# Performance work log

Measured on AMD Instinct MI355X. Metric: run time of the kernel, lower is better.

## Reference

```python
import jax, jax.numpy as jnp
import numpy as np

NUM_NODES = 100000
NUM_FEATURES = 64
HIDDEN = 128
NUM_CLASSES = 2
N_CLIQUES = 500000
CLIQUE_SIZE = 4


def setup_inputs() -> dict:
    key = jax.random.key(0)
    k = jax.random.split(key, 8)
    x = jax.random.normal(k[0], (NUM_NODES, NUM_FEATURES), dtype=jnp.float32)
    cliques_r = jax.random.randint(k[1], (N_CLIQUES, CLIQUE_SIZE), 0, NUM_NODES)
    cliques_s = jax.random.randint(k[2], (N_CLIQUES, CLIQUE_SIZE), 0, NUM_NODES)
    # learned parameters
    node_features = jax.random.normal(k[3], (NUM_NODES, NUM_FEATURES), dtype=jnp.float32)
    W5 = jax.random.normal(k[4], (NUM_FEATURES, HIDDEN), dtype=jnp.float32) / np.sqrt(NUM_FEATURES)
    b5 = jnp.zeros((HIDDEN,), dtype=jnp.float32)
    W6 = jax.random.normal(k[5], (HIDDEN, NUM_CLASSES), dtype=jnp.float32) / np.sqrt(HIDDEN)
    b6 = jnp.zeros((NUM_CLASSES,), dtype=jnp.float32)
    return {"x": x, "cliques_r": cliques_r, "cliques_s": cliques_s,
            "node_features": node_features, "W5": W5, "b5": b5, "W6": W6, "b6": b6}


def _edge_pred(node_features, cliques, W5, b5, W6, b6):
    # EdgePredNet: edge_index = positions 0..k-1, so x_i = clique node 0, x_j = clique node 1.
    x_i = node_features[cliques[:, 0]]  # [N, F] irregular gather
    x_j = node_features[cliques[:, 1]]  # [N, F]
    h = jax.nn.relu((x_i * x_j) @ W5 + b5)  # [N, H]
    logits = h @ W6 + b6  # [N, C]
    return jax.nn.softmax(logits, axis=-1)


def reference(x, cliques_r, cliques_s, node_features, W5, b5, W6, b6):
    # forward ignores the x argument: x = self.node_features
    probs_r = _edge_pred(node_features, cliques_r, W5, b5, W6, b6)           # [Nr, C]
    probs_s = _edge_pred(node_features, cliques_s, W5, b5, W6, b6)[:, None]  # [Ns, 1, C] (stacked singleton lists)
    return probs_r, probs_s
```

## Files before the change

### kernel.cpp

```cpp
#include <hip/hip_runtime.h>
#include <hip/hip_bf16.h>
#include <hip/hip_fp16.h>

typedef _Float16 half8 __attribute__((ext_vector_type(8)));
typedef float    f32x4 __attribute__((ext_vector_type(4)));

#define NCLQ      500000
#define NF        64
#define HID       128
#define NTILES    62500
#define RTILES    31250
#define NFH_ELEMS 6400000

__global__ __launch_bounds__(256) void cvt_kernel(const float* __restrict__ nf,
                                                  const float* __restrict__ w5,
                                                  _Float16* __restrict__ nfh,
                                                  _Float16* __restrict__ w5h)
{
    const long id = (long)blockIdx.x * blockDim.x + threadIdx.x;
    const long NCHUNK = NFH_ELEMS / 8;
    const long WCHUNK = (NF * HID) / 8;
    const float* src; _Float16* dst; long c;
    if (id < NCHUNK)                { src = nf; dst = nfh; c = id; }
    else if (id < NCHUNK + WCHUNK)  { src = w5; dst = w5h; c = id - NCHUNK; }
    else return;
    const float4 u = ((const float4*)src)[c * 2 + 0];
    const float4 v = ((const float4*)src)[c * 2 + 1];
    half8 h;
    h[0] = (_Float16)u.x; h[1] = (_Float16)u.y; h[2] = (_Float16)u.z; h[3] = (_Float16)u.w;
    h[4] = (_Float16)v.x; h[5] = (_Float16)v.y; h[6] = (_Float16)v.z; h[7] = (_Float16)v.w;
    ((half8*)dst)[c] = h;
}

template <int PRE>
__global__ __launch_bounds__(256, 4) void edge_pred_kernel(
    const float*    __restrict__ nf,
    const _Float16* __restrict__ nfh,
    const int*      __restrict__ cr,
    const int*      __restrict__ cs,
    const float*    __restrict__ w5,
    const _Float16* __restrict__ w5h,
    const float*    __restrict__ b5,
    const float*    __restrict__ w6,
    const float*    __restrict__ b6,
    float*          __restrict__ out)
{
    const int lane = threadIdx.x & 63;
    const int wid  = threadIdx.x >> 6;
    const int i    = lane & 15;
    const int g    = lane >> 4;

    half8 bfrag[8][2];
    float b5r[8], wdr[8];
#pragma unroll
    for (int t = 0; t < 8; ++t) {
        const int col = 16 * t + i;
        b5r[t] = b5[col];
        wdr[t] = w6[2 * col] - w6[2 * col + 1];
#pragma unroll
        for (int kb = 0; kb < 2; ++kb) {
            half8 f;
#pragma unroll
            for (int e = 0; e < 8; ++e) {
                const int k = 32 * kb + 8 * g + e;
                f[e] = PRE ? w5h[k * HID + col] : (_Float16)w5[k * HID + col];
            }
            bfrag[t][kb] = f;
        }
    }
    const float bdiff = b6[0] - b6[1];

    const int gw = blockIdx.x * 4 + wid;
    const int nw = gridDim.x * 4;
    if (gw >= NTILES) return;

    auto clq = [&](int T) -> int2 {
        T = (T < NTILES) ? T : (NTILES - 1);
        const bool is_r = (T < RTILES);
        const int* cl   = is_r ? cr : cs;
        const long e    = (long)(is_r ? T : T - RTILES) * 16 + i;
        return *(const int2*)(cl + e * 4);
    };
    auto gather = [&](int2 idx, half8& d0a, half8& d0b, half8& d1a, half8& d1b) {
        if constexpr (PRE) {
            const _Float16* p0 = nfh + (long)idx.x * NF;
            const _Float16* p1 = nfh + (long)idx.y * NF;
            d0a = *(const half8*)(p0 + 8 * g);
            d0b = *(const half8*)(p0 + 32 + 8 * g);
            d1a = *(const half8*)(p1 + 8 * g);
            d1b = *(const half8*)(p1 + 32 + 8 * g);
        } else {
            const float* p0 = nf + (long)idx.x * NF;
            const float* p1 = nf + (long)idx.y * NF;
            const float4 xa = *(const float4*)(p0 + 8 * g);
            const float4 xb = *(const float4*)(p0 + 8 * g + 4);
            const float4 ya = *(const float4*)(p1 + 8 * g);
            const float4 yb = *(const float4*)(p1 + 8 * g + 4);
            const float4 xc = *(const float4*)(p0 + 32 + 8 * g);
            const float4 xd = *(const float4*)(p0 + 32 + 8 * g + 4);
            const float4 yc = *(const float4*)(p1 + 32 + 8 * g);
            const float4 yd = *(const float4*)(p1 + 32 + 8 * g + 4);
            d0a[0]=(_Float16)xa.x; d0a[1]=(_Float16)xa.y; d0a[2]=(_Float16)xa.z; d0a[3]=(_Float16)xa.w;
            d0a[4]=(_Float16)xb.x; d0a[5]=(_Float16)xb.y; d0a[6]=(_Float16)xb.z; d0a[7]=(_Float16)xb.w;
            d0b[0]=(_Float16)xc.x; d0b[1]=(_Float16)xc.y; d0b[2]=(_Float16)xc.z; d0b[3]=(_Float16)xc.w;
            d0b[4]=(_Float16)xd.x; d0b[5]=(_Float16)xd.y; d0b[6]=(_Float16)xd.z; d0b[7]=(_Float16)xd.w;
            d1a[0]=(_Float16)ya.x; d1a[1]=(_Float16)ya.y; d1a[2]=(_Float16)ya.z; d1a[3]=(_Float16)ya.w;
            d1a[4]=(_Float16)yb.x; d1a[5]=(_Float16)yb.y; d1a[6]=(_Float16)yb.z; d1a[7]=(_Float16)yb.w;
            d1b[0]=(_Float16)yc.x; d1b[1]=(_Float16)yc.y; d1b[2]=(_Float16)yc.z; d1b[3]=(_Float16)yc.w;
            d1b[4]=(_Float16)yd.x; d1b[5]=(_Float16)yd.y; d1b[6]=(_Float16)yd.z; d1b[7]=(_Float16)yd.w;
        }
    };

    int2 idxA = clq(gw);
    half8 d0a, d0b, d1a, d1b;
    gather(idxA, d0a, d0b, d1a, d1b);
    int2 idxB = clq(gw + nw);

    for (int tile = gw; tile < NTILES; tile += nw) {
        const int2 idxC = clq(tile + 2 * nw);
        half8 e0a, e0b, e1a, e1b;
        gather(idxB, e0a, e0b, e1a, e1b);

        const half8 a0 = d0a * d1a;
        const half8 a1 = d0b * d1b;

        f32x4 acc[8];
#pragma unroll
        for (int t = 0; t < 8; ++t) {
            f32x4 z = {0.f, 0.f, 0.f, 0.f};
            z = __builtin_amdgcn_mfma_f32_16x16x32_f16(a0, bfrag[t][0], z, 0, 0, 0);
            z = __builtin_amdgcn_mfma_f32_16x16x32_f16(a1, bfrag[t][1], z, 0, 0, 0);
            acc[t] = z;
        }

        float s0, s1, s2, s3;
#pragma unroll
        for (int r = 0; r < 4; ++r) {
            float a = 0.f;
#pragma unroll
            for (int t = 0; t < 8; ++t) {
                float h = acc[t][r] + b5r[t];
                h = fmaxf(h, 0.f);
                a = fmaf(h, wdr[t], a);
            }
            a += __shfl_xor(a, 1);
            a += __shfl_xor(a, 2);
            a += __shfl_xor(a, 4);
            a += __shfl_xor(a, 8);
            if (r == 0) s0 = a; else if (r == 1) s1 = a; else if (r == 2) s2 = a; else s3 = a;
        }

        if (i < 8) {
            const int r = i >> 1, c = i & 1;
            const float sv = (r == 0) ? s0 : (r == 1) ? s1 : (r == 2) ? s2 : s3;
            const float z  = sv + bdiff;
            const float pz = 1.0f / (1.0f + __expf(-z));
            out[(long)tile * 32 + 8 * g + i] = c ? (1.0f - pz) : pz;
        }

        d0a = e0a; d0b = e0b; d1a = e1a; d1b = e1b;
        idxB = idxC;
    }
}

extern "C" void kernel_launch(void* const* d_in, const int* in_sizes, int n_in,
                              void* d_out, int out_size, void* d_ws, size_t ws_size,
                              hipStream_t stream) {
    const float* nf = (const float*)d_in[3];
    const int*   cr = (const int*)d_in[1];
    const int*   cs = (const int*)d_in[2];
    const float* w5 = (const float*)d_in[4];
    const float* b5 = (const float*)d_in[5];
    const float* w6 = (const float*)d_in[6];
    const float* b6 = (const float*)d_in[7];
    float* out = (float*)d_out;

    const size_t need = (size_t)NFH_ELEMS * 2 + (size_t)NF * HID * 2;
    if (ws_size >= need) {
        _Float16* nfh = (_Float16*)d_ws;
        _Float16* w5h = (_Float16*)((char*)d_ws + (size_t)NFH_ELEMS * 2);
        const int cvt_blocks = (NFH_ELEMS / 8 + NF * HID / 8 + 255) / 256;
        hipLaunchKernelGGL(cvt_kernel, dim3(cvt_blocks), dim3(256), 0, stream,
                           nf, w5, nfh, w5h);
        hipLaunchKernelGGL((edge_pred_kernel<1>), dim3(1024), dim3(256), 0, stream,
                           nf, nfh, cr, cs, w5, w5h, b5, w6, b6, out);
    } else {
        hipLaunchKernelGGL((edge_pred_kernel<0>), dim3(1024), dim3(256), 0, stream,
                           nf, (const _Float16*)nullptr, cr, cs, w5,
                           (const _Float16*)nullptr, b5, w6, b6, out);
    }
}
```

Baseline: 62.55 us.

## Process two clique tiles per wave and stage W5 fragments in LDS

Each wave now handles a pair of 16-clique tiles per iteration, issuing 8 gathers at once and interleaving two MFMA chains, with the ReLU/W6 reduction fused into the MFMA loop. The W5 B-fragments are converted once per block into shared memory and read from LDS each iteration, no longer held in 64 registers. The separate W5 fp16 conversion in the cvt kernel is dropped. This aims for more memory-level parallelism and lower register pressure, at the cost of LDS reads per tile and a block-level sync at startup.

```diff
diff --git a/kernel.cpp b/kernel.cpp
--- a/kernel.cpp
+++ b/kernel.cpp
@@ -1,35 +1,26 @@
 #include <hip/hip_runtime.h>
-#include <hip/hip_bf16.h>
 #include <hip/hip_fp16.h>
 
 typedef _Float16 half8 __attribute__((ext_vector_type(8)));
 typedef float    f32x4 __attribute__((ext_vector_type(4)));
 
-#define NCLQ      500000
 #define NF        64
 #define HID       128
-#define NTILES    62500
-#define RTILES    31250
+#define NPAIRS    31250
+#define RPAIRS    15625
 #define NFH_ELEMS 6400000
 
 __global__ __launch_bounds__(256) void cvt_kernel(const float* __restrict__ nf,
-                                                  const float* __restrict__ w5,
-                                                  _Float16* __restrict__ nfh,
-                                                  _Float16* __restrict__ w5h)
+                                                  _Float16* __restrict__ nfh)
 {
-    const long id = (long)blockIdx.x * blockDim.x + threadIdx.x;
-    const long NCHUNK = NFH_ELEMS / 8;
-    const long WCHUNK = (NF * HID) / 8;
-    const float* src; _Float16* dst; long c;
-    if (id < NCHUNK)                { src = nf; dst = nfh; c = id; }
-    else if (id < NCHUNK + WCHUNK)  { src = w5; dst = w5h; c = id - NCHUNK; }
-    else return;
-    const float4 u = ((const float4*)src)[c * 2 + 0];
-    const float4 v = ((const float4*)src)[c * 2 + 1];
+    const long id = (long)blockIdx.x * 256 + threadIdx.x;
+    if (id >= NFH_ELEMS / 8) return;
+    const float4 u = ((const float4*)nf)[id * 2 + 0];
+    const float4 v = ((const float4*)nf)[id * 2 + 1];
     half8 h;
     h[0] = (_Float16)u.x; h[1] = (_Float16)u.y; h[2] = (_Float16)u.z; h[3] = (_Float16)u.w;
     h[4] = (_Float16)v.x; h[5] = (_Float16)v.y; h[6] = (_Float16)v.z; h[7] = (_Float16)v.w;
-    ((half8*)dst)[c] = h;
+    ((half8*)nfh)[id] = h;
 }
 
 template <int PRE>
@@ -39,127 +30,144 @@
     const int*      __restrict__ cr,
     const int*      __restrict__ cs,
     const float*    __restrict__ w5,
-    const _Float16* __restrict__ w5h,
     const float*    __restrict__ b5,
     const float*    __restrict__ w6,
     const float*    __restrict__ b6,
     float*          __restrict__ out)
 {
-    const int lane = threadIdx.x & 63;
-    const int wid  = threadIdx.x >> 6;
+    __shared__ _Float16 lfrag[16][64][8];
+
+    const int tid  = threadIdx.x;
+    const int lane = tid & 63;
+    const int wid  = tid >> 6;
     const int i    = lane & 15;
     const int g    = lane >> 4;
 
-    half8 bfrag[8][2];
+    {
+        const int l = tid & 63, fb = tid >> 6;
+        const int li = l & 15, lg = l >> 4;
+        for (int f = fb; f < 16; f += 4) {
+            const int t = f >> 1, kb = f & 1;
+            const int col = 16 * t + li;
+            half8 v;
+#pragma unroll
+            for (int e = 0; e < 8; ++e)
+                v[e] = (_Float16)w5[(32 * kb + 8 * lg + e) * HID + col];
+            *(half8*)&lfrag[f][l][0] = v;
+        }
+    }
+    __syncthreads();
+
     float b5r[8], wdr[8];
 #pragma unroll
     for (int t = 0; t < 8; ++t) {
         const int col = 16 * t + i;
         b5r[t] = b5[col];
         wdr[t] = w6[2 * col] - w6[2 * col + 1];
-#pragma unroll
-        for (int kb = 0; kb < 2; ++kb) {
-            half8 f;
-#pragma unroll
-            for (int e = 0; e < 8; ++e) {
-                const int k = 32 * kb + 8 * g + e;
-                f[e] = PRE ? w5h[k * HID + col] : (_Float16)w5[k * HID + col];
-            }
-            bfrag[t][kb] = f;
-        }
     }
     const float bdiff = b6[0] - b6[1];
 
     const int gw = blockIdx.x * 4 + wid;
     const int nw = gridDim.x * 4;
-    if (gw >= NTILES) return;
+    if (gw >= NPAIRS) return;
 
-    auto clq = [&](int T) -> int2 {
-        T = (T < NTILES) ? T : (NTILES - 1);
-        const bool is_r = (T < RTILES);
-        const int* cl   = is_r ? cr : cs;
-        const long e    = (long)(is_r ? T : T - RTILES) * 16 + i;
-        return *(const int2*)(cl + e * 4);
+    auto clqpair = [&](int p, int2& c0, int2& c1) {
+        p = (p < NPAIRS) ? p : (NPAIRS - 1);
+        const int* cl  = (p < RPAIRS) ? cr : cs;
+        const long e0  = (long)((p < RPAIRS) ? p : p - RPAIRS) * 32 + i;
+        c0 = *(const int2*)(cl + e0 * 4);
+        c1 = *(const int2*)(cl + (e0 + 16) * 4);
     };
-    auto gather = [&](int2 idx, half8& d0a, half8& d0b, half8& d1a, half8& d1b) {
+    auto gather1 = [&](int2 ix, half8& x0, half8& x1, half8& y0, half8& y1) {
         if constexpr (PRE) {
-            const _Float16* p0 = nfh + (long)idx.x * NF;
-            const _Float16* p1 = nfh + (long)idx.y * NF;
-            d0a = *(const half8*)(p0 + 8 * g);
-            d0b = *(const half8*)(p0 + 32 + 8 * g);
-            d1a = *(const half8*)(p1 + 8 * g);
-            d1b = *(const half8*)(p1 + 32 + 8 * g);
+            const _Float16* p0 = nfh + (long)ix.x * NF;
+            const _Float16* p1 = nfh + (long)ix.y * NF;
+            x0 = *(const half8*)(p0 + 8 * g);
+            x1 = *(const half8*)(p0 + 32 + 8 * g);
+            y0 = *(const half8*)(p1 + 8 * g);
+            y1 = *(const half8*)(p1 + 32 + 8 * g);
         } else {
-            const float* p0 = nf + (long)idx.x * NF;
-            const float* p1 = nf + (long)idx.y * NF;
-            const float4 xa = *(const float4*)(p0 + 8 * g);
-            const float4 xb = *(const float4*)(p0 + 8 * g + 4);
-            const float4 ya = *(const float4*)(p1 + 8 * g);
-            const float4 yb = *(const float4*)(p1 + 8 * g + 4);
-            const float4 xc = *(const float4*)(p0 + 32 + 8 * g);
-            const float4 xd = *(const float4*)(p0 + 32 + 8 * g + 4);
-            const float4 yc = *(const float4*)(p1 + 32 + 8 * g);
-            const float4 yd = *(const float4*)(p1 + 32 + 8 * g + 4);
-            d0a[0]=(_Float16)xa.x; d0a[1]=(_Float16)xa.y; d0a[2]=(_Float16)xa.z; d0a[3]=(_Float16)xa.w;
-            d0a[4]=(_Float16)xb.x; d0a[5]=(_Float16)xb.y; d0a[6]=(_Float16)xb.z; d0a[7]=(_Float16)xb.w;
-            d0b[0]=(_Float16)xc.x; d0b[1]=(_Float16)xc.y; d0b[2]=(_Float16)xc.z; d0b[3]=(_Float16)xc.w;
-            d0b[4]=(_Float16)xd.x; d0b[5]=(_Float16)xd.y; d0b[6]=(_Float16)xd.z; d0b[7]=(_Float16)xd.w;
-            d1a[0]=(_Float16)ya.x; d1a[1]=(_Float16)ya.y; d1a[2]=(_Float16)ya.z; d1a[3]=(_Float16)ya.w;
-            d1a[4]=(_Float16)yb.x; d1a[5]=(_Float16)yb.y; d1a[6]=(_Float16)yb.z; d1a[7]=(_Float16)yb.w;
-            d1b[0]=(_Float16)yc.x; d1b[1]=(_Float16)yc.y; d1b[2]=(_Float16)yc.z; d1b[3]=(_Float16)yc.w;
-            d1b[4]=(_Float16)yd.x; d1b[5]=(_Float16)yd.y; d1b[6]=(_Float16)yd.z; d1b[7]=(_Float16)yd.w;
+            const float* p0 = nf + (long)ix.x * NF;
+            const float* p1 = nf + (long)ix.y * NF;
+            const float4 a = *(const float4*)(p0 + 8 * g);
+            const float4 b = *(const float4*)(p0 + 8 * g + 4);
+            const float4 c = *(const float4*)(p0 + 32 + 8 * g);
+            const float4 d = *(const float4*)(p0 + 32 + 8 * g + 4);
+            const float4 e = *(const float4*)(p1 + 8 * g);
+            const float4 f = *(const float4*)(p1 + 8 * g + 4);
+            const float4 m = *(const float4*)(p1 + 32 + 8 * g);
+            const float4 n = *(const float4*)(p1 + 32 + 8 * g + 4);
+            x0[0]=(_Float16)a.x; x0[1]=(_Float16)a.y; x0[2]=(_Float16)a.z; x0[3]=(_Float16)a.w;
+            x0[4]=(_Float16)b.x; x0[5]=(_Float16)b.y; x0[6]=(_Float16)b.z; x0[7]=(_Float16)b.w;
+            x1[0]=(_Float16)c.x; x1[1]=(_Float16)c.y; x1[2]=(_Float16)c.z; x1[3]=(_Float16)c.w;
+            x1[4]=(_Float16)d.x; x1[5]=(_Float16)d.y; x1[6]=(_Float16)d.z; x1[7]=(_Float16)d.w;
+            y0[0]=(_Float16)e.x; y0[1]=(_Float16)e.y; y0[2]=(_Float16)e.z; y0[3]=(_Float16)e.w;
+            y0[4]=(_Float16)f.x; y0[5]=(_Float16)f.y; y0[6]=(_Float16)f.z; y0[7]=(_Float16)f.w;
+            y1[0]=(_Float16)m.x; y1[1]=(_Float16)m.y; y1[2]=(_Float16)m.z; y1[3]=(_Float16)m.w;
+            y1[4]=(_Float16)n.x; y1[5]=(_Float16)n.y; y1[6]=(_Float16)n.z; y1[7]=(_Float16)n.w;
         }
     };
 
-    int2 idxA = clq(gw);
-    half8 d0a, d0b, d1a, d1b;
-    gather(idxA, d0a, d0b, d1a, d1b);
-    int2 idxB = clq(gw + nw);
+    int2 ix0, ix1, ixn0, ixn1;
+    half8 d[8];
+    clqpair(gw, ix0, ix1);
+    gather1(ix0, d[0], d[1], d[2], d[3]);
+    gather1(ix1, d[4], d[5], d[6], d[7]);
+    clqpair(gw + nw, ixn0, ixn1);
 
-    for (int tile = gw; tile < NTILES; tile += nw) {
-        const int2 idxC = clq(tile + 2 * nw);
-        half8 e0a, e0b, e1a, e1b;
-        gather(idxB, e0a, e0b, e1a, e1b);
+    for (int p = gw; p < NPAIRS; p += nw) {
+        const half8 a00 = d[0] * d[2];
+        const half8 a01 = d[1] * d[3];
+        const half8 a10 = d[4] * d[6];
+        const half8 a11 = d[5] * d[7];
 
-        const half8 a0 = d0a * d1a;
-        const half8 a1 = d0b * d1b;
+        gather1(ixn0, d[0], d[1], d[2], d[3]);
+        gather1(ixn1, d[4], d[5], d[6], d[7]);
+        clqpair(p + 2 * nw, ixn0, ixn1);
 
-        f32x4 acc[8];
+        float su[2][4] = {{0.f,0.f,0.f,0.f},{0.f,0.f,0.f,0.f}};
 #pragma unroll
         for (int t = 0; t < 8; ++t) {
-            f32x4 z = {0.f, 0.f, 0.f, 0.f};
-            z = __builtin_amdgcn_mfma_f32_16x16x32_f16(a0, bfrag[t][0], z, 0, 0, 0);
-            z = __builtin_amdgcn_mfma_f32_16x16x32_f16(a1, bfrag[t][1], z, 0, 0, 0);
-            acc[t] = z;
+            const half8 bf0 = *(const half8*)&lfrag[2 * t + 0][lane][0];
+            const half8 bf1 = *(const half8*)&lfrag[2 * t + 1][lane][0];
+            f32x4 z0 = {0.f,0.f,0.f,0.f}, z1 = {0.f,0.f,0.f,0.f};
+            z0 = __builtin_amdgcn_mfma_f32_16x16x32_f16(a00, bf0, z0, 0, 0, 0);
+            z0 = __builtin_amdgcn_mfma_f32_16x16x32_f16(a01, bf1, z0, 0, 0, 0);
+            z1 = __builtin_amdgcn_mfma_f32_16x16x32_f16(a10, bf0, z1, 0, 0, 0);
+            z1 = __builtin_amdgcn_mfma_f32_16x16x32_f16(a11, bf1, z1, 0, 0, 0);
+#pragma unroll
+            for (int r = 0; r < 4; ++r) {
+                const float h0 = fmaxf(z0[r] + b5r[t], 0.f);
+                const float h1 = fmaxf(z1[r] + b5r[t], 0.f);
+                su[0][r] = fmaf(h0, wdr[t], su[0][r]);
+                su[1][r] = fmaf(h1, wdr[t], su[1][r]);
+            }
         }
 
-        float s0, s1, s2, s3;
 #pragma unroll
-        for (int r = 0; r < 4; ++r) {
-            float a = 0.f;
+        for (int u = 0; u < 2; ++u)
 #pragma unroll
-            for (int t = 0; t < 8; ++t) {
-                float h = acc[t][r] + b5r[t];
-                h = fmaxf(h, 0.f);
-                a = fmaf(h, wdr[t], a);
+            for (int r = 0; r < 4; ++r) {
+                float a_ = su[u][r];
+                a_ += __shfl_xor(a_, 1);
+                a_ += __shfl_xor(a_, 2);
+                a_ += __shfl_xor(a_, 4);
+                a_ += __shfl_xor(a_, 8);
+                su[u][r] = a_;
             }
-            a += __shfl_xor(a, 1);
-            a += __shfl_xor(a, 2);
-            a += __shfl_xor(a, 4);
-            a += __shfl_xor(a, 8);
-            if (r == 0) s0 = a; else if (r == 1) s1 = a; else if (r == 2) s2 = a; else s3 = a;
-        }
 
         if (i < 8) {
             const int r = i >> 1, c = i & 1;
-            const float sv = (r == 0) ? s0 : (r == 1) ? s1 : (r == 2) ? s2 : s3;
-            const float z  = sv + bdiff;
-            const float pz = 1.0f / (1.0f + __expf(-z));
-            out[(long)tile * 32 + 8 * g + i] = c ? (1.0f - pz) : pz;
+#pragma unroll
+            for (int u = 0; u < 2; ++u) {
+                const float sv = (r == 0) ? su[u][0] : (r == 1) ? su[u][1]
+                               : (r == 2) ? su[u][2] : su[u][3];
+                const float z  = sv + bdiff;
+                const float pz = 1.0f / (1.0f + __expf(-z));
+                const long tile = 2L * p + u;
+                out[tile * 32 + 8 * g + i] = c ? (1.0f - pz) : pz;
+            }
         }
-
-        d0a = e0a; d0b = e0b; d1a = e1a; d1b = e1b;
-        idxB = idxC;
     }
 }
 
@@ -175,18 +183,14 @@
     const float* b6 = (const float*)d_in[7];
     float* out = (float*)d_out;
 
-    const size_t need = (size_t)NFH_ELEMS * 2 + (size_t)NF * HID * 2;
-    if (ws_size >= need) {
+    if (ws_size >= (size_t)NFH_ELEMS * 2) {
         _Float16* nfh = (_Float16*)d_ws;
-        _Float16* w5h = (_Float16*)((char*)d_ws + (size_t)NFH_ELEMS * 2);
-        const int cvt_blocks = (NFH_ELEMS / 8 + NF * HID / 8 + 255) / 256;
-        hipLaunchKernelGGL(cvt_kernel, dim3(cvt_blocks), dim3(256), 0, stream,
-                           nf, w5, nfh, w5h);
+        hipLaunchKernelGGL(cvt_kernel, dim3(NFH_ELEMS / 8 / 256), dim3(256), 0, stream,
+                           nf, nfh);
         hipLaunchKernelGGL((edge_pred_kernel<1>), dim3(1024), dim3(256), 0, stream,
-                           nf, nfh, cr, cs, w5, w5h, b5, w6, b6, out);
+                           nf, nfh, cr, cs, w5, b5, w6, b6, out);
     } else {
         hipLaunchKernelGGL((edge_pred_kernel<0>), dim3(1024), dim3(256), 0, stream,
-                           nf, (const _Float16*)nullptr, cr, cs, w5,
-                           (const _Float16*)nullptr, b5, w6, b6, out);
+                           nf, (const _Float16*)nullptr, cr, cs, w5, b5, w6, b6, out);
     }
 }
```

Result: slower. 104.9 us (+67.8%).
